# Performance work log

Hardware: AMD Instinct MI355X
Metric: run time of the kernel (lower is better)

The kernel has to match this reference:

```python
import jax, jax.numpy as jnp
import numpy as np

V, L, H, D, DFF = 32000, 6, 8, 64, 1024
DM = H * D  # 512
N, T = 4, 1024
EPS = 1e-3  # keras LayerNormalization default epsilon


def setup_inputs() -> dict:
    key = jax.random.key(0)
    ks = jax.random.split(key, 13)
    s = 0.02
    return {
        "x": jax.random.randint(ks[0], (N, T), 0, V, dtype=jnp.int32),
        "emb": jax.random.normal(ks[1], (V, DM), jnp.float32) * s,
        "Wqkv": jax.random.normal(ks[2], (L, DM, 3 * DM), jnp.float32) * s,
        "bqkv": jnp.zeros((L, 3 * DM), jnp.float32),
        "Wff": jax.random.normal(ks[3], (L, DM, DFF), jnp.float32) * s,
        "bff": jnp.zeros((L, DFF), jnp.float32),
        "Wo": jax.random.normal(ks[4], (L, DFF, DM), jnp.float32) * s,
        "bo": jnp.zeros((L, DM), jnp.float32),
        "g1": jnp.ones((L, DM), jnp.float32),
        "beta1": jnp.zeros((L, DM), jnp.float32),
        "g2": jnp.ones((L, DM), jnp.float32),
        "beta2": jnp.zeros((L, DM), jnp.float32),
    }


def _pos_encoding(seq_len, d_model):
    pos = jnp.arange(seq_len, dtype=jnp.float32)[:, None]
    i = jnp.arange(d_model, dtype=jnp.float32)[None, :]
    angle_rates = 1.0 / jnp.power(10000.0, 2.0 * jnp.floor(i / 2.0) / d_model)
    ang = pos * angle_rates
    even = (jnp.arange(d_model) % 2) == 0
    return jnp.where(even[None, :], jnp.sin(ang), jnp.cos(ang))  # [T, DM]


def _ln(x, g, b):
    m = jnp.mean(x, axis=-1, keepdims=True)
    v = jnp.mean(jnp.square(x - m), axis=-1, keepdims=True)
    return g * (x - m) / jnp.sqrt(v + EPS) + b


def reference(x, emb, Wqkv, bqkv, Wff, bff, Wo, bo, g1, beta1, g2, beta2):
    n, t = x.shape
    h = emb[x] * jnp.sqrt(jnp.float32(DM))          # [N,T,DM]
    h = h + _pos_encoding(t, DM)[None, :, :]
    # causal additive mask: 1 above diagonal, 0 on/below
    mask = 1.0 - jnp.tril(jnp.ones((t, t), jnp.float32))
    neg = mask[None, None, :, :] * -1e9
    scale = 1.0 / jnp.sqrt(jnp.float32(D))
    for l in range(L):
        qkv = h @ Wqkv[l] + bqkv[l]                 # [N,T,3*DM]
        qkv = qkv.reshape(n, t, H, D, 3)
        q, k, v = [jnp.transpose(qkv[..., j], (0, 2, 1, 3)) for j in range(3)]  # [N,H,T,D]
        logits = jnp.einsum("nhtd,nhsd->nhts", q, k) * scale + neg
        w = jax.nn.softmax(logits, axis=-1)
        a = jnp.einsum("nhts,nhsd->nhtd", w, v)     # [N,H,T,D]
        a = jnp.transpose(a, (0, 2, 1, 3)).reshape(n, t, DM)
        h = _ln(h + a, g1[l], beta1[l])
        ff = jax.nn.relu(h @ Wff[l] + bff[l]) @ Wo[l] + bo[l]
        h = _ln(h + ff, g2[l], beta2[l])
    return h
```

## Files before the change

### kernel.cpp

```cpp
#include <hip/hip_runtime.h>
#include <hip/hip_bf16.h>
#include <math.h>

#define DM   512
#define TT   1024
#define NB   4
#define NHD  8
#define LAYERS 6
#define DFFD 1024
#define MROWS (NB*TT)
#define PERBUF (NB*NHD*TT*64)

typedef __bf16 bf16x8 __attribute__((ext_vector_type(8)));
typedef __bf16 bf16x4 __attribute__((ext_vector_type(4)));
typedef float f32x4 __attribute__((ext_vector_type(4)));

__device__ __forceinline__ void gl_lds16(const __bf16* g, __bf16* l) {
    __builtin_amdgcn_global_load_lds((const __attribute__((address_space(1))) void*)g,
                                     (__attribute__((address_space(3))) void*)l, 16, 0, 0);
}

__global__ __launch_bounds__(256) void embed_pos_kernel(const int* __restrict__ x,
    const float* __restrict__ emb, float* __restrict__ h, __bf16* __restrict__ hb)
{
    int row = blockIdx.x;
    int t = row & (TT - 1);
    int tok = x[row];
    const float* e = emb + (size_t)tok * DM;
    float* out = h + (size_t)row * DM;
    __bf16* outb = hb + (size_t)row * DM;
    for (int i = threadIdx.x; i < DM; i += 256) {
        float val = e[i] * 22.62741699796952f;
        int pair = i >> 1;
        float rate = powf(10000.0f, -(float)pair * (1.0f / 256.0f));
        float ang = (float)t * rate;
        float pe = (i & 1) ? cosf(ang) : sinf(ang);
        float v = val + pe;
        out[i] = v;
        outb[i] = (__bf16)v;
    }
}

__global__ __launch_bounds__(256) void convert_all_kernel(
    const float* __restrict__ Wqkv, const float* __restrict__ Wff, const float* __restrict__ Wo,
    const float* __restrict__ bqkv,
    __bf16* __restrict__ WtQ, __bf16* __restrict__ WtF, __bf16* __restrict__ WtO,
    float* __restrict__ bqkv_p)
{
    __shared__ float tile[32][33];
    int l = blockIdx.z;
    int t = blockIdx.x;
    const float* W; __bf16* Wt; int K, N, bx, by; bool perm = false;
    if (t < 768)       { W = Wqkv; Wt = WtQ; K = 512;  N = 1536; bx = t & 15;  by = t >> 4; perm = true; }
    else if (t < 1280) { int u = t - 768;  W = Wff; Wt = WtF; K = 512;  N = 1024; bx = u & 15; by = u >> 4; }
    else               { int u = t - 1280; W = Wo;  Wt = WtO; K = 1024; N = 512;  bx = u & 31; by = u >> 5; }
    int k0 = bx * 32, n0 = by * 32;
    const float* Wl = W + (size_t)l * K * N;
    __bf16* Wtl = Wt + (size_t)l * K * N;
    int tx = threadIdx.x & 31, ty = threadIdx.x >> 5;
    #pragma unroll
    for (int i = ty; i < 32; i += 8)
        tile[i][tx] = Wl[(size_t)(k0 + i) * N + n0 + tx];
    if (perm && bx == 0 && ty == 0) {
        int c = n0 + tx;
        bqkv_p[l * 1536 + (c % 3) * 512 + c / 3] = bqkv[(size_t)l * 1536 + c];
    }
    __syncthreads();
    #pragma unroll
    for (int i = ty; i < 32; i += 8) {
        int c = n0 + i;
        int row = perm ? ((c % 3) * 512 + c / 3) : c;
        Wtl[(size_t)row * K + k0 + tx] = (__bf16)tile[tx][i];
    }
}

template<int BM, int BN, int MODE>
__global__ __launch_bounds__(256) void gemm2p(const __bf16* __restrict__ A,
    const __bf16* __restrict__ Bt, const float* __restrict__ bias,
    void* __restrict__ Cv, int M, int Nc, int K)
{
    constexpr int WM = BM / 2, WN = BN / 2;
    constexpr int MT = WM / 16, NT = WN / 16;
    constexpr int ACH = BM / 64;
    constexpr int BCH = BN / 64;
    __shared__ __align__(16) __bf16 As[2][BM * 32];
    __shared__ __align__(16) __bf16 Bs[2][BN * 32];
    int tid = threadIdx.x;
    int lane = tid & 63;
    int wave = tid >> 6;
    int ln = lane & 15, q = lane >> 4;
    int wrow = (wave >> 1) * WM, wcol = (wave & 1) * WN;
    int n0 = blockIdx.x * BN, m0 = blockIdx.y * BM;

    f32x4 acc[MT][NT] = {};

    const __bf16* Ab = A + (size_t)m0 * K;
    const __bf16* Bb = Bt + (size_t)n0 * K;
    int srow = lane >> 2;
    int scol = (lane & 3) * 8;

    const __bf16* Aga[ACH];
    const __bf16* Bga[BCH];
    #pragma unroll
    for (int i = 0; i < ACH; i++)
        Aga[i] = Ab + (size_t)(wave * (16 * ACH) + 16 * i + srow) * K + scol;
    #pragma unroll
    for (int i = 0; i < BCH; i++)
        Bga[i] = Bb + (size_t)(wave * (16 * BCH) + 16 * i + srow) * K + scol;

    auto STAGE = [&](int kp, int buf) {
        #pragma unroll
        for (int i = 0; i < ACH; i++)
            gl_lds16(Aga[i] + kp, As[buf] + (wave * (16 * ACH) + 16 * i) * 32);
        #pragma unroll
        for (int i = 0; i < BCH; i++)
            gl_lds16(Bga[i] + kp, Bs[buf] + (wave * (16 * BCH) + 16 * i) * 32);
    };
    auto COMPUTE = [&](int buf) {
        bf16x8 af[MT], bfr[NT];
        #pragma unroll
        for (int mt = 0; mt < MT; mt++)
            af[mt] = *(const bf16x8*)&As[buf][(wrow + mt * 16 + ln) * 32 + q * 8];
        #pragma unroll
        for (int nt = 0; nt < NT; nt++)
            bfr[nt] = *(const bf16x8*)&Bs[buf][(wcol + nt * 16 + ln) * 32 + q * 8];
        #pragma unroll
        for (int mt = 0; mt < MT; mt++)
            #pragma unroll
            for (int nt = 0; nt < NT; nt++)
                acc[mt][nt] = __builtin_amdgcn_mfma_f32_16x16x32_bf16(af[mt], bfr[nt], acc[mt][nt], 0, 0, 0);
    };

    STAGE(0, 0);
    __syncthreads();
    int kp = 0;
    for (; kp + 64 < K; kp += 64) {
        STAGE(kp + 32, 1);
        COMPUTE(0);
        __syncthreads();
        STAGE(kp + 64, 0);
        COMPUTE(1);
        __syncthreads();
    }
    STAGE(kp + 32, 1);
    COMPUTE(0);
    __syncthreads();
    COMPUTE(1);

    #pragma unroll
    for (int mt = 0; mt < MT; mt++) {
        int mbase = m0 + wrow + mt * 16 + q * 4;
        if constexpr (MODE == 0) {
            float* C = (float*)Cv;
            #pragma unroll
            for (int r = 0; r < 4; r++) {
                int m = mbase + r;
                #pragma unroll
                for (int nt = 0; nt < NT; nt++) {
                    int c = n0 + wcol + nt * 16 + ln;
                    C[(size_t)m * Nc + c] = acc[mt][nt][r] + bias[c];
                }
            }
        } else if constexpr (MODE == 1) {
            __bf16* Cb = (__bf16*)Cv;
            #pragma unroll
            for (int r = 0; r < 4; r++) {
                int m = mbase + r;
                #pragma unroll
                for (int nt = 0; nt < NT; nt++) {
                    int c = n0 + wcol + nt * 16 + ln;
                    float val = acc[mt][nt][r] + bias[c];
                    Cb[(size_t)m * Nc + c] = (__bf16)fmaxf(val, 0.f);
                }
            }
        } else {
            __bf16* Cb = (__bf16*)Cv;
            int n = mbase >> 10, t = mbase & (TT - 1);
            #pragma unroll
            for (int nt = 0; nt < NT; nt++) {
                int c = n0 + wcol + nt * 16 + ln;
                int buf = c >> 9;
                int hd = c & 511;
                int hh = hd >> 6, d = hd & 63;
                float bv = bias[c];
                if (buf == 2) {
                    size_t idx = 2 * (size_t)PERBUF + (((size_t)(n * NHD + hh) * 64 + d) << 10) + t;
                    bf16x4 v4;
                    #pragma unroll
                    for (int r = 0; r < 4; r++) v4[r] = (__bf16)(acc[mt][nt][r] + bv);
                    *(bf16x4*)&Cb[idx] = v4;
                } else {
                    size_t base = (size_t)buf * PERBUF + (((size_t)(n * NHD + hh) * TT + t) << 6) + d;
                    #pragma unroll
                    for (int r = 0; r < 4; r++)
                        Cb[base + (size_t)(r << 6)] = (__bf16)(acc[mt][nt][r] + bv);
                }
            }
        }
    }
}

#define PPAD 72
#define NCHUNK 40
__global__ __launch_bounds__(256) void attn_partial_kernel(const __bf16* __restrict__ qb,
    const __bf16* __restrict__ kb, const __bf16* __restrict__ vtb,
    float* __restrict__ po, float* __restrict__ pden)
{
    __shared__ __align__(16) __bf16 Ksh[64 * 64];
    __shared__ __align__(16) __bf16 Vsh[2][64 * 64];
    __shared__ __align__(16) __bf16 Ps[64 * PPAD];

    int u = (NCHUNK - 1) - blockIdx.x;
    int nh = blockIdx.y;
    int g, off;
    if (u < 4)       { g = 0; off = 0;  }
    else if (u < 12) { g = 1; off = 4;  }
    else if (u < 24) { g = 2; off = 12; }
    else             { g = 3; off = 24; }
    int rem = u - off;
    int nper = g + 1;
    int qq = rem / nper;
    int c  = rem - qq * nper;
    int qt = g * 4 + qq;
    int st0 = c * 4;
    int st1 = min(st0 + 4, qt + 1);

    int tid = threadIdx.x;
    int lane = tid & 63, w = tid >> 6;
    int ln = lane & 15, q = lane >> 4;

    const __bf16* Kg = kb + (size_t)nh * TT * 64;
    const __bf16* Vg = vtb + (size_t)nh * 64 * TT;

    const __bf16* Qrow = qb + ((size_t)nh * TT + (size_t)qt * 64 + w * 16 + ln) * 64;
    bf16x8 aq0 = *(const bf16x8*)(Qrow + q * 8);
    bf16x8 aq1 = *(const bf16x8*)(Qrow + 32 + q * 8);

    int srow = lane >> 3;
    int swz  = ((lane & 7) ^ srow) << 3;
    int r0 = (w * 2 + 0) * 8 + srow;
    int r1 = (w * 2 + 1) * 8 + srow;
    const __bf16* Kg0 = Kg + (size_t)r0 * 64 + swz;
    const __bf16* Kg1 = Kg + (size_t)r1 * 64 + swz;
    const __bf16* Vg0 = Vg + (size_t)r0 * TT + swz;
    const __bf16* Vg1 = Vg + (size_t)r1 * TT + swz;
    __bf16* Kd0 = Ksh + (w * 2 + 0) * 512;
    __bf16* Kd1 = Ksh + (w * 2 + 1) * 512;

    f32x4 o_acc[4] = {};
    float den_lane = 0.f;
    int qrow_l = w * 16 + ln;

    int cur = 0;
    gl_lds16(Kg0 + st0 * 4096, Kd0);
    gl_lds16(Kg1 + st0 * 4096, Kd1);
    gl_lds16(Vg0 + st0 * 64, Vsh[0] + (w * 2 + 0) * 512);
    gl_lds16(Vg1 + st0 * 64, Vsh[0] + (w * 2 + 1) * 512);

    int kswz = ln & 7;
    for (int st = st0; st < st1; st++) {
        __syncthreads();

        f32x4 st_acc[4] = {};
        #pragma unroll
        for (int mt = 0; mt < 4; mt++) {
            int r = mt * 16 + ln;
            bf16x8 k0v = *(const bf16x8*)&Ksh[r * 64 + ((q ^ kswz) << 3)];
            st_acc[mt] = __builtin_amdgcn_mfma_f32_16x16x32_bf16(k0v, aq0, st_acc[mt], 0, 0, 0);
            bf16x8 k1v = *(const bf16x8*)&Ksh[r * 64 + (((q + 4) ^ kswz) << 3)];
            st_acc[mt] = __builtin_amdgcn_mfma_f32_16x16x32_bf16(k1v, aq1, st_acc[mt], 0, 0, 0);
        }

        bool diag = (st == qt);
        #pragma unroll
        for (int mt = 0; mt < 4; mt++) {
            int s0i = mt * 16 + q * 4;
            bf16x4 p4;
            #pragma unroll
            for (int r = 0; r < 4; r++) {
                float p;
                if (diag && (s0i + r) > qrow_l) p = 0.f;
                else p = exp2f(st_acc[mt][r] * 0.18033688011112042f);
                den_lane += p;
                p4[r] = (__bf16)p;
            }
            *(bf16x4*)&Ps[qrow_l * PPAD + s0i] = p4;
        }
        __syncthreads();

        if (st + 1 < st1) {
            gl_lds16(Kg0 + (st + 1) * 4096, Kd0);
            gl_lds16(Kg1 + (st + 1) * 4096, Kd1);
            gl_lds16(Vg0 + (st + 1) * 64, Vsh[cur ^ 1] + (w * 2 + 0) * 512);
            gl_lds16(Vg1 + (st + 1) * 64, Vsh[cur ^ 1] + (w * 2 + 1) * 512);
        }

        #pragma unroll
        for (int ks = 0; ks < 2; ks++) {
            bf16x8 af = *(const bf16x8*)&Vsh[cur][(w * 16 + ln) * 64 + (((ks * 4 + q) ^ kswz) << 3)];
            #pragma unroll
            for (int nt = 0; nt < 4; nt++) {
                bf16x8 bfr = *(const bf16x8*)&Ps[(nt * 16 + ln) * PPAD + ks * 32 + q * 8];
                o_acc[nt] = __builtin_amdgcn_mfma_f32_16x16x32_bf16(af, bfr, o_acc[nt], 0, 0, 0);
            }
        }
        cur ^= 1;
    }

    den_lane += __shfl_xor(den_lane, 16, 64);
    den_lane += __shfl_xor(den_lane, 32, 64);
    size_t slot = (size_t)nh * NCHUNK + u;
    if (lane < 16)
        pden[slot * 64 + qrow_l] = den_lane;

    #pragma unroll
    for (int nt = 0; nt < 4; nt++)
        *(f32x4*)&po[(slot << 12) + (size_t)(nt * 16 + ln) * 64 + w * 16 + q * 4] = o_acc[nt];
}

__global__ __launch_bounds__(256) void add_ln_attn_kernel(float* __restrict__ h,
    __bf16* __restrict__ hb, const float* __restrict__ po, const float* __restrict__ pden,
    const float* __restrict__ g, const float* __restrict__ b)
{
    int w = threadIdx.x >> 6, lane = threadIdx.x & 63;
    int row = (blockIdx.x << 2) + w;
    int n = row >> 10, t = row & (TT - 1);
    int qt = t >> 6, qrow = t & 63;
    int gg = qt >> 2, nc = gg + 1;
    const int offs[4] = {0, 4, 12, 24};
    int u0 = offs[gg] + (qt - gg * 4) * nc;
    int hh = lane >> 3;
    int d0 = (lane & 7) * 8;
    size_t s0 = (size_t)(n * NHD + hh) * NCHUNK + u0;

    f32x4 a0 = {0.f,0.f,0.f,0.f}, a1 = {0.f,0.f,0.f,0.f};
    float den = 0.f;
    for (int c = 0; c < nc; c++) {
        const float* p = po + ((s0 + c) << 12) + (size_t)qrow * 64 + d0;
        a0 += *(const f32x4*)p;
        a1 += *(const f32x4*)(p + 4);
        den += pden[(s0 + c) * 64 + qrow];
    }
    float inv = 1.0f / den;

    size_t base = (size_t)row * DM + lane * 8;
    f32x4 x0 = *(const f32x4*)&h[base];
    f32x4 x1 = *(const f32x4*)&h[base + 4];
    x0 += a0 * inv;
    x1 += a1 * inv;

    float s1 = x0[0]+x0[1]+x0[2]+x0[3] + x1[0]+x1[1]+x1[2]+x1[3];
    float s2 = x0[0]*x0[0]+x0[1]*x0[1]+x0[2]*x0[2]+x0[3]*x0[3]
             + x1[0]*x1[0]+x1[1]*x1[1]+x1[2]*x1[2]+x1[3]*x1[3];
    #pragma unroll
    for (int m = 1; m < 64; m <<= 1) {
        s1 += __shfl_xor(s1, m, 64);
        s2 += __shfl_xor(s2, m, 64);
    }
    float mean = s1 * (1.0f / 512.0f);
    float var = s2 * (1.0f / 512.0f) - mean * mean;
    float rstd = rsqrtf(var + 1e-3f);

    f32x4 gg0 = *(const f32x4*)&g[lane * 8];
    f32x4 gg1 = *(const f32x4*)&g[lane * 8 + 4];
    f32x4 bb0 = *(const f32x4*)&b[lane * 8];
    f32x4 bb1 = *(const f32x4*)&b[lane * 8 + 4];
    f32x4 o0, o1;
    bf16x8 pb;
    #pragma unroll
    for (int i = 0; i < 4; i++) {
        o0[i] = gg0[i] * ((x0[i] - mean) * rstd) + bb0[i];
        o1[i] = gg1[i] * ((x1[i] - mean) * rstd) + bb1[i];
        pb[i] = (__bf16)o0[i];
        pb[4 + i] = (__bf16)o1[i];
    }
    *(f32x4*)&h[base] = o0;
    *(f32x4*)&h[base + 4] = o1;
    *(bf16x8*)(hb + base) = pb;
}

__global__ __launch_bounds__(256) void add_ln_kernel(float* __restrict__ h,
    __bf16* __restrict__ hb, const float* __restrict__ a,
    const float* __restrict__ g, const float* __restrict__ b)
{
    int w = threadIdx.x >> 6, lane = threadIdx.x & 63;
    int row = (blockIdx.x << 2) + w;
    size_t base4 = (size_t)row * (DM / 4);
    const float4* h4 = (const float4*)h;
    const float4* a4 = (const float4*)a;
    float4 x0 = h4[base4 + lane];
    float4 x1 = h4[base4 + 64 + lane];
    float4 y0 = a4[base4 + lane];
    float4 y1 = a4[base4 + 64 + lane];
    x0.x += y0.x; x0.y += y0.y; x0.z += y0.z; x0.w += y0.w;
    x1.x += y1.x; x1.y += y1.y; x1.z += y1.z; x1.w += y1.w;
    float s1 = x0.x + x0.y + x0.z + x0.w + x1.x + x1.y + x1.z + x1.w;
    float s2 = x0.x*x0.x + x0.y*x0.y + x0.z*x0.z + x0.w*x0.w
             + x1.x*x1.x + x1.y*x1.y + x1.z*x1.z + x1.w*x1.w;
    #pragma unroll
    for (int m = 1; m < 64; m <<= 1) {
        s1 += __shfl_xor(s1, m, 64);
        s2 += __shfl_xor(s2, m, 64);
    }
    float mean = s1 * (1.0f / 512.0f);
    float var = s2 * (1.0f / 512.0f) - mean * mean;
    float rstd = rsqrtf(var + 1e-3f);
    const float4* g4 = (const float4*)g;
    const float4* b4 = (const float4*)b;
    float4 gg0 = g4[lane], gg1 = g4[64 + lane];
    float4 bb0 = b4[lane], bb1 = b4[64 + lane];
    float4 o0, o1;
    o0.x = gg0.x * ((x0.x - mean) * rstd) + bb0.x;
    o0.y = gg0.y * ((x0.y - mean) * rstd) + bb0.y;
    o0.z = gg0.z * ((x0.z - mean) * rstd) + bb0.z;
    o0.w = gg0.w * ((x0.w - mean) * rstd) + bb0.w;
    o1.x = gg1.x * ((x1.x - mean) * rstd) + bb1.x;
    o1.y = gg1.y * ((x1.y - mean) * rstd) + bb1.y;
    o1.z = gg1.z * ((x1.z - mean) * rstd) + bb1.z;
    o1.w = gg1.w * ((x1.w - mean) * rstd) + bb1.w;
    ((float4*)h)[base4 + lane] = o0;
    ((float4*)h)[base4 + 64 + lane] = o1;
    bf16x4 p0, p1;
    p0[0] = (__bf16)o0.x; p0[1] = (__bf16)o0.y; p0[2] = (__bf16)o0.z; p0[3] = (__bf16)o0.w;
    p1[0] = (__bf16)o1.x; p1[1] = (__bf16)o1.y; p1[2] = (__bf16)o1.z; p1[3] = (__bf16)o1.w;
    *(bf16x4*)(hb + (size_t)row * DM + lane * 4) = p0;
    *(bf16x4*)(hb + (size_t)row * DM + 256 + lane * 4) = p1;
}

extern "C" void kernel_launch(void* const* d_in, const int* in_sizes, int n_in,
                              void* d_out, int out_size, void* d_ws, size_t ws_size,
                              hipStream_t stream) {
    const int*   x     = (const int*)d_in[0];
    const float* emb   = (const float*)d_in[1];
    const float* Wqkv  = (const float*)d_in[2];
    const float* bqkv  = (const float*)d_in[3];
    const float* Wff   = (const float*)d_in[4];
    const float* bff   = (const float*)d_in[5];
    const float* Wo    = (const float*)d_in[6];
    const float* bo    = (const float*)d_in[7];
    const float* g1    = (const float*)d_in[8];
    const float* beta1 = (const float*)d_in[9];
    const float* g2    = (const float*)d_in[10];
    const float* beta2 = (const float*)d_in[11];

    float* h = (float*)d_out;
    char* w = (char*)d_ws;
    __bf16* qkvb = (__bf16*)w;
    __bf16* ffb  = (__bf16*)w;
    float*  abuf = (float*)(w + 25165824);
    __bf16* hb   = (__bf16*)(w + 33554432);
    __bf16* WtQ  = (__bf16*)(w + 37748736);
    __bf16* WtF  = (__bf16*)(w + 47185920);
    __bf16* WtO  = (__bf16*)(w + 53477376);
    float*  po   = (float*)(w + 59768832);
    float*  pden = (float*)(w + 80740352);
    float*  bqkv_p = (float*)(w + 81068032);

    convert_all_kernel<<<dim3(1792, 1, LAYERS), 256, 0, stream>>>(
        Wqkv, Wff, Wo, bqkv, WtQ, WtF, WtO, bqkv_p);

    embed_pos_kernel<<<MROWS, 256, 0, stream>>>(x, emb, h, hb);

    for (int l = 0; l < LAYERS; l++) {
        const float* bff_l  = bff  + (size_t)l * DFFD;
        const float* bo_l   = bo   + (size_t)l * DM;

        gemm2p<128, 64, 2><<<dim3(24, 32), 256, 0, stream>>>(
            hb, WtQ + (size_t)l * 1536 * 512, bqkv_p + l * 1536, qkvb, MROWS, 3 * DM, 512);

        attn_partial_kernel<<<dim3(NCHUNK, NB * NHD), 256, 0, stream>>>(
            qkvb, qkvb + PERBUF, qkvb + 2 * (size_t)PERBUF, po, pden);

        add_ln_attn_kernel<<<MROWS / 4, 256, 0, stream>>>(
            h, hb, po, pden, g1 + l * DM, beta1 + l * DM);

        gemm2p<128, 64, 1><<<dim3(16, 32), 256, 0, stream>>>(
            hb, WtF + (size_t)l * 1024 * 512, bff_l, ffb, MROWS, DFFD, 512);

        gemm2p<64, 64, 0><<<dim3(8, 64), 256, 0, stream>>>(
            ffb, WtO + (size_t)l * 512 * 1024, bo_l, abuf, MROWS, DM, 1024);

        add_ln_kernel<<<MROWS / 4, 256, 0, stream>>>(h, hb, abuf, g2 + l * DM, beta2 + l * DM);
    }
}
```

Before: 638.8 us.

## Rebalance causal attention split into 24 chunks of at most eight key tiles

Replaces the 40-chunk causal attention decomposition (up to four key tiles per chunk, up to four partials per query tile) with a table-driven 24-chunk schedule. Each query tile is split into at most two chunks of roughly equal size, ordered largest first. The combine kernel now reads at most two partials instead of up to four. This cuts partial-result traffic and the number of blocks, in exchange for longer per-block work and fewer blocks to fill the GPU.

After: 631.4 us. About the same (-1.2%).

```diff
diff --git a/kernel.cpp b/kernel.cpp
--- a/kernel.cpp
+++ b/kernel.cpp
@@ -19,6 +19,13 @@
     __builtin_amdgcn_global_load_lds((const __attribute__((address_space(1))) void*)g,
                                      (__attribute__((address_space(3))) void*)l, 16, 0, 0);
 }
+
+__constant__ signed char C_QT[24]  = {15,15,14, 7,14,13,13,12, 6,12,11,11,10, 5,10, 9, 9, 8, 4, 8, 3, 2, 1, 0};
+__constant__ signed char C_ST0[24] = { 0, 8, 0, 0, 8, 0, 7, 0, 0, 7, 0, 6, 0, 0, 6, 0, 5, 0, 0, 5, 0, 0, 0, 0};
+__constant__ signed char C_ST1[24] = { 8,16, 8, 8,15, 7,14, 7, 7,13, 6,12, 6, 6,11, 5,10, 5, 5, 9, 4, 3, 2, 1};
+__constant__ unsigned char C_UA[16] = {23,22,21,20,18,13,8,3,17,15,12,10,7,5,2,0};
+__constant__ unsigned char C_UB[16] = { 0, 0, 0, 0, 0, 0,0,0,19,16,14,11,9,6,4,1};
+#define NCHUNK 24
 
 __global__ __launch_bounds__(256) void embed_pos_kernel(const int* __restrict__ x,
     const float* __restrict__ emb, float* __restrict__ h, __bf16* __restrict__ hb)
@@ -201,7 +208,6 @@
 }
 
 #define PPAD 72
-#define NCHUNK 40
 __global__ __launch_bounds__(256) void attn_partial_kernel(const __bf16* __restrict__ qb,
     const __bf16* __restrict__ kb, const __bf16* __restrict__ vtb,
     float* __restrict__ po, float* __restrict__ pden)
@@ -210,20 +216,11 @@
     __shared__ __align__(16) __bf16 Vsh[2][64 * 64];
     __shared__ __align__(16) __bf16 Ps[64 * PPAD];
 
-    int u = (NCHUNK - 1) - blockIdx.x;
+    int u = blockIdx.x;
     int nh = blockIdx.y;
-    int g, off;
-    if (u < 4)       { g = 0; off = 0;  }
-    else if (u < 12) { g = 1; off = 4;  }
-    else if (u < 24) { g = 2; off = 12; }
-    else             { g = 3; off = 24; }
-    int rem = u - off;
-    int nper = g + 1;
-    int qq = rem / nper;
-    int c  = rem - qq * nper;
-    int qt = g * 4 + qq;
-    int st0 = c * 4;
-    int st1 = min(st0 + 4, qt + 1);
+    int qt  = C_QT[u];
+    int st0 = C_ST0[u];
+    int st1 = C_ST1[u];
 
     int tid = threadIdx.x;
     int lane = tid & 63, w = tid >> 6;
@@ -326,20 +323,21 @@
     int row = (blockIdx.x << 2) + w;
     int n = row >> 10, t = row & (TT - 1);
     int qt = t >> 6, qrow = t & 63;
-    int gg = qt >> 2, nc = gg + 1;
-    const int offs[4] = {0, 4, 12, 24};
-    int u0 = offs[gg] + (qt - gg * 4) * nc;
     int hh = lane >> 3;
     int d0 = (lane & 7) * 8;
-    size_t s0 = (size_t)(n * NHD + hh) * NCHUNK + u0;
-
-    f32x4 a0 = {0.f,0.f,0.f,0.f}, a1 = {0.f,0.f,0.f,0.f};
-    float den = 0.f;
-    for (int c = 0; c < nc; c++) {
-        const float* p = po + ((s0 + c) << 12) + (size_t)qrow * 64 + d0;
-        a0 += *(const f32x4*)p;
-        a1 += *(const f32x4*)(p + 4);
-        den += pden[(s0 + c) * 64 + qrow];
+    size_t base_nh = (size_t)(n * NHD + hh) * NCHUNK;
+
+    size_t sa = base_nh + C_UA[qt];
+    const float* pa = po + (sa << 12) + (size_t)qrow * 64 + d0;
+    f32x4 a0 = *(const f32x4*)pa;
+    f32x4 a1 = *(const f32x4*)(pa + 4);
+    float den = pden[sa * 64 + qrow];
+    if (qt >= 8) {
+        size_t sb = base_nh + C_UB[qt];
+        const float* pb2 = po + (sb << 12) + (size_t)qrow * 64 + d0;
+        a0 += *(const f32x4*)pb2;
+        a1 += *(const f32x4*)(pb2 + 4);
+        den += pden[sb * 64 + qrow];
     }
     float inv = 1.0f / den;
 
```
